# Optimization experiments

Measured on AMD Instinct MI355X. Metric: run time of the kernel, lower is better.

The kernel has to match this reference:

```python
import jax, jax.numpy as jnp
import numpy as np

LAMB = 0.01
ROOT_GAMMA = 2 * LAMB    # 0.02
COARSE_GAMMA = 4 * LAMB  # 0.04
FINE_GAMMA = 6 * LAMB    # 0.06
NUM_FINE = 100000
FEAT_DIM = 512
NUM_COARSE = 100


def setup_inputs() -> dict:
    key = jax.random.key(0)
    k1, k2, k3 = jax.random.split(key, 3)
    fc_weights = jax.random.normal(k1, (NUM_FINE, FEAT_DIM), dtype=jnp.float32)
    fc_bias = jax.random.normal(k2, (NUM_FINE,), dtype=jnp.float32)
    coarse_map = jax.random.randint(k3, (NUM_FINE,), 0, NUM_COARSE, dtype=jnp.int32)
    return {"fc_weights": fc_weights, "fc_bias": fc_bias, "coarse_map": coarse_map}


def reference(fc_weights, fc_bias, coarse_map):
    # Per-row sum of squares of weights + bias: [NUM_FINE]
    # torch.norm(x)**2 == sum(x**2), so each group's contribution is
    # gamma * sum of row_sq over the group's rows.
    row_sq = jnp.sum(fc_weights * fc_weights, axis=1) + fc_bias * fc_bias

    # Root group: all rows.
    root_term = ROOT_GAMMA * jnp.sum(row_sq)

    # Coarse groups: rows sharing a coarse label (irregular segment reduce).
    coarse_sums = jax.ops.segment_sum(row_sq, coarse_map, num_segments=NUM_COARSE)
    coarse_term = COARSE_GAMMA * jnp.sum(coarse_sums)

    # Fine groups: each row is its own singleton group.
    fine_term = FINE_GAMMA * jnp.sum(row_sq)

    return root_term + coarse_term + fine_term
```

## Files before the change

kernel.cpp:

```cpp
#include <hip/hip_runtime.h>


constexpr int BLOCK = 256;
constexpr int GRID1 = 2048;

__device__ __forceinline__ float block_reduce(float acc) {
    #pragma unroll
    for (int off = 32; off > 0; off >>= 1)
        acc += __shfl_down(acc, off, 64);
    __shared__ float smem[BLOCK / 64];
    const int lane = threadIdx.x & 63;
    const int wave = threadIdx.x >> 6;
    if (lane == 0) smem[wave] = acc;
    __syncthreads();
    float s = 0.f;
    if (threadIdx.x == 0) {
        #pragma unroll
        for (int w = 0; w < BLOCK / 64; ++w) s += smem[w];
    }
    return s;
}

__global__ __launch_bounds__(BLOCK) void sq_partial_kernel(
    const float* __restrict__ w, long long nw,
    const float* __restrict__ b, long long nb,
    float* __restrict__ partials)
{
    const long long tid    = (long long)blockIdx.x * blockDim.x + threadIdx.x;
    const long long stride = (long long)gridDim.x * blockDim.x;

    float acc = 0.f;

    const long long nw4 = nw >> 2;
    const float4* w4 = reinterpret_cast<const float4*>(w);
    for (long long i = tid; i < nw4; i += stride) {
        float4 v = w4[i];
        acc = fmaf(v.x, v.x, acc);
        acc = fmaf(v.y, v.y, acc);
        acc = fmaf(v.z, v.z, acc);
        acc = fmaf(v.w, v.w, acc);
    }
    for (long long i = (nw4 << 2) + tid; i < nw; i += stride)
        acc = fmaf(w[i], w[i], acc);

    const long long nb4 = nb >> 2;
    const float4* b4 = reinterpret_cast<const float4*>(b);
    for (long long i = tid; i < nb4; i += stride) {
        float4 v = b4[i];
        acc = fmaf(v.x, v.x, acc);
        acc = fmaf(v.y, v.y, acc);
        acc = fmaf(v.z, v.z, acc);
        acc = fmaf(v.w, v.w, acc);
    }
    for (long long i = (nb4 << 2) + tid; i < nb; i += stride)
        acc = fmaf(b[i], b[i], acc);

    float s = block_reduce(acc);
    if (threadIdx.x == 0) partials[blockIdx.x] = s;
}

__global__ __launch_bounds__(BLOCK) void final_kernel(
    const float* __restrict__ partials, int n, float* __restrict__ out)
{
    float acc = 0.f;
    for (int i = threadIdx.x; i < n; i += BLOCK) acc += partials[i];
    float s = block_reduce(acc);
    if (threadIdx.x == 0) out[0] = 0.12f * s;
}

extern "C" void kernel_launch(void* const* d_in, const int* in_sizes, int n_in,
                              void* d_out, int out_size, void* d_ws, size_t ws_size,
                              hipStream_t stream) {
    const float* w = (const float*)d_in[0];
    const float* b = (const float*)d_in[1];

    const long long nw = (long long)in_sizes[0];
    const long long nb = (long long)in_sizes[1];

    float* partials = (float*)d_ws;
    float* out = (float*)d_out;

    sq_partial_kernel<<<GRID1, BLOCK, 0, stream>>>(w, nw, b, nb, partials);
    final_kernel<<<1, BLOCK, 0, stream>>>(partials, GRID1, out);
}
```

Before: 273.7 us.

## Fuse final reduction via last-block atomic counter and unroll loads fourfold

```diff
diff --git a/kernel.cpp b/kernel.cpp
--- a/kernel.cpp
+++ b/kernel.cpp
@@ -2,70 +2,79 @@
 
 
 constexpr int BLOCK = 256;
-constexpr int GRID1 = 2048;
+constexpr int GRID  = 2048;
 
-__device__ __forceinline__ float block_reduce(float acc) {
+__global__ __launch_bounds__(BLOCK) void grouplasso_fused(
+    const float4* __restrict__ w4, long long nw4,
+    const float4* __restrict__ b4, long long nb4,
+    float* partials, unsigned int* counter, float* out)
+{
+    const long long stride = (long long)GRID * BLOCK;
+    const long long tid    = (long long)blockIdx.x * BLOCK + threadIdx.x;
+
+    float a0 = 0.f, a1 = 0.f, a2 = 0.f, a3 = 0.f;
+
+    long long i = tid;
+    for (; i + 3 * stride < nw4; i += 4 * stride) {
+        float4 v0 = w4[i];
+        float4 v1 = w4[i + stride];
+        float4 v2 = w4[i + 2 * stride];
+        float4 v3 = w4[i + 3 * stride];
+        a0 = fmaf(v0.x, v0.x, a0); a0 = fmaf(v0.y, v0.y, a0);
+        a0 = fmaf(v0.z, v0.z, a0); a0 = fmaf(v0.w, v0.w, a0);
+        a1 = fmaf(v1.x, v1.x, a1); a1 = fmaf(v1.y, v1.y, a1);
+        a1 = fmaf(v1.z, v1.z, a1); a1 = fmaf(v1.w, v1.w, a1);
+        a2 = fmaf(v2.x, v2.x, a2); a2 = fmaf(v2.y, v2.y, a2);
+        a2 = fmaf(v2.z, v2.z, a2); a2 = fmaf(v2.w, v2.w, a2);
+        a3 = fmaf(v3.x, v3.x, a3); a3 = fmaf(v3.y, v3.y, a3);
+        a3 = fmaf(v3.z, v3.z, a3); a3 = fmaf(v3.w, v3.w, a3);
+    }
+    for (; i < nw4; i += stride) {
+        float4 v = w4[i];
+        a0 = fmaf(v.x, v.x, a0); a0 = fmaf(v.y, v.y, a0);
+        a0 = fmaf(v.z, v.z, a0); a0 = fmaf(v.w, v.w, a0);
+    }
+    for (long long j = tid; j < nb4; j += stride) {
+        float4 v = b4[j];
+        a1 = fmaf(v.x, v.x, a1); a1 = fmaf(v.y, v.y, a1);
+        a1 = fmaf(v.z, v.z, a1); a1 = fmaf(v.w, v.w, a1);
+    }
+
+    float acc = (a0 + a1) + (a2 + a3);
+
+    __shared__ float smem[BLOCK / 64];
+    __shared__ int is_last;
     #pragma unroll
     for (int off = 32; off > 0; off >>= 1)
         acc += __shfl_down(acc, off, 64);
-    __shared__ float smem[BLOCK / 64];
     const int lane = threadIdx.x & 63;
     const int wave = threadIdx.x >> 6;
     if (lane == 0) smem[wave] = acc;
     __syncthreads();
-    float s = 0.f;
+
     if (threadIdx.x == 0) {
+        float s = smem[0] + smem[1] + smem[2] + smem[3];
+        __hip_atomic_store(&partials[blockIdx.x], s,
+                           __ATOMIC_RELEASE, __HIP_MEMORY_SCOPE_AGENT);
+        unsigned prev = __hip_atomic_fetch_add(counter, 1u,
+                           __ATOMIC_ACQ_REL, __HIP_MEMORY_SCOPE_AGENT);
+        is_last = (prev == (unsigned)(GRID - 1));
+    }
+    __syncthreads();
+
+    if (is_last) {
+        float f = 0.f;
+        for (int t = threadIdx.x; t < GRID; t += BLOCK)
+            f += __hip_atomic_load(&partials[t],
+                                   __ATOMIC_ACQUIRE, __HIP_MEMORY_SCOPE_AGENT);
         #pragma unroll
-        for (int w = 0; w < BLOCK / 64; ++w) s += smem[w];
+        for (int off = 32; off > 0; off >>= 1)
+            f += __shfl_down(f, off, 64);
+        if (lane == 0) smem[wave] = f;
+        __syncthreads();
+        if (threadIdx.x == 0)
+            out[0] = 0.12f * (smem[0] + smem[1] + smem[2] + smem[3]);
     }
-    return s;
-}
-
-__global__ __launch_bounds__(BLOCK) void sq_partial_kernel(
-    const float* __restrict__ w, long long nw,
-    const float* __restrict__ b, long long nb,
-    float* __restrict__ partials)
-{
-    const long long tid    = (long long)blockIdx.x * blockDim.x + threadIdx.x;
-    const long long stride = (long long)gridDim.x * blockDim.x;
-
-    float acc = 0.f;
-
-    const long long nw4 = nw >> 2;
-    const float4* w4 = reinterpret_cast<const float4*>(w);
-    for (long long i = tid; i < nw4; i += stride) {
-        float4 v = w4[i];
-        acc = fmaf(v.x, v.x, acc);
-        acc = fmaf(v.y, v.y, acc);
-        acc = fmaf(v.z, v.z, acc);
-        acc = fmaf(v.w, v.w, acc);
-    }
-    for (long long i = (nw4 << 2) + tid; i < nw; i += stride)
-        acc = fmaf(w[i], w[i], acc);
-
-    const long long nb4 = nb >> 2;
-    const float4* b4 = reinterpret_cast<const float4*>(b);
-    for (long long i = tid; i < nb4; i += stride) {
-        float4 v = b4[i];
-        acc = fmaf(v.x, v.x, acc);
-        acc = fmaf(v.y, v.y, acc);
-        acc = fmaf(v.z, v.z, acc);
-        acc = fmaf(v.w, v.w, acc);
-    }
-    for (long long i = (nb4 << 2) + tid; i < nb; i += stride)
-        acc = fmaf(b[i], b[i], acc);
-
-    float s = block_reduce(acc);
-    if (threadIdx.x == 0) partials[blockIdx.x] = s;
-}
-
-__global__ __launch_bounds__(BLOCK) void final_kernel(
-    const float* __restrict__ partials, int n, float* __restrict__ out)
-{
-    float acc = 0.f;
-    for (int i = threadIdx.x; i < n; i += BLOCK) acc += partials[i];
-    float s = block_reduce(acc);
-    if (threadIdx.x == 0) out[0] = 0.12f * s;
 }
 
 extern "C" void kernel_launch(void* const* d_in, const int* in_sizes, int n_in,
@@ -74,12 +83,14 @@
     const float* w = (const float*)d_in[0];
     const float* b = (const float*)d_in[1];
 
-    const long long nw = (long long)in_sizes[0];
-    const long long nb = (long long)in_sizes[1];
+    const long long nw4 = (long long)in_sizes[0] >> 2;
+    const long long nb4 = (long long)in_sizes[1] >> 2;
 
-    float* partials = (float*)d_ws;
+    unsigned int* counter = (unsigned int*)d_ws;
+    float* partials = (float*)((char*)d_ws + 256);
     float* out = (float*)d_out;
 
-    sq_partial_kernel<<<GRID1, BLOCK, 0, stream>>>(w, nw, b, nb, partials);
-    final_kernel<<<1, BLOCK, 0, stream>>>(partials, GRID1, out);
+    hipMemsetAsync(counter, 0, sizeof(unsigned int), stream);
+    grouplasso_fused<<<GRID, BLOCK, 0, stream>>>(
+        (const float4*)w, nw4, (const float4*)b, nb4, partials, counter, out);
 }
```

Result: slower. 458.3 us (+67.4%).
